# Kernel optimization log

Measured on AMD Instinct MI355X. Metric: run time of the kernel, lower is better.

The kernel has to match this reference:

```python
import jax, jax.numpy as jnp
import numpy as np

N = 50000      # nodes
E = 250000     # edges
NG = 2500      # graphs
H = 32         # atom_dim
ND = 32        # node feature dim
ED = 16        # edge feature dim
CONV_N = 3     # message passing steps
EMB_STEPS = 3  # Set2Set processing steps


def setup_inputs() -> dict:
    key = jax.random.key(0)
    ks = jax.random.split(key, 16)
    w = lambda k, shape, s=0.05: jax.random.normal(k, shape, jnp.float32) * s
    return {
        "x": jax.random.normal(ks[0], (N, ND), jnp.float32),
        "edge_index": jax.random.randint(ks[1], (2, E), 0, N),
        "edge_attr": jax.random.normal(ks[2], (E, ED), jnp.float32),
        "batch": jnp.sort(jax.random.randint(ks[3], (N,), 0, NG)),
        "lin_w": w(ks[4], (ND, H)), "lin_b": jnp.zeros((H,), jnp.float32),
        "e_w1": w(ks[5], (ED, 2 * H)), "e_b1": jnp.zeros((2 * H,), jnp.float32),
        "e_w2": w(ks[6], (2 * H, H * H)), "e_b2": jnp.zeros((H * H,), jnp.float32),
        "gru_w_ih": w(ks[7], (3 * H, H)), "gru_w_hh": w(ks[8], (3 * H, H)),
        "gru_b_ih": jnp.zeros((3 * H,), jnp.float32), "gru_b_hh": jnp.zeros((3 * H,), jnp.float32),
        "lstm_w_ih": w(ks[9], (4 * H, 2 * H)), "lstm_w_hh": w(ks[10], (4 * H, H)),
        "lstm_b_ih": jnp.zeros((4 * H,), jnp.float32), "lstm_b_hh": jnp.zeros((4 * H,), jnp.float32),
        "pred_w": w(ks[11], (2 * H, 1)), "pred_b": jnp.zeros((1,), jnp.float32),
    }


def _mpnn_forward(x, edge_attr, lin_w, lin_b, e_w1, e_b1, e_w2, e_b2,
                  gru_w_ih, gru_w_hh, gru_b_ih, gru_b_hh,
                  lstm_w_ih, lstm_w_hh, lstm_b_ih, lstm_b_hh,
                  pred_w, pred_b, edge_index, batch):
    src, dst = edge_index[0], edge_index[1]
    # initial node embedding: relu(Linear(node_dim -> atom_dim))
    out = jax.nn.relu(x @ lin_w + lin_b)            # [N, H]
    h = out                                         # GRU hidden state [N, H]

    # edge-conditioned weights (edge MLP output is constant across conv steps)
    e_h = jax.nn.relu(edge_attr @ e_w1 + e_b1)      # [E, 2H]
    W_e = (e_h @ e_w2 + e_b2).reshape(E, H, H)      # [E, H, H]

    # mean-aggregation denominator per target node
    deg = jax.ops.segment_sum(jnp.ones((E,), out.dtype), dst, num_segments=N)
    denom = jnp.maximum(deg, 1.0)[:, None]          # [N, 1]

    for _ in range(CONV_N):
        # NNConv message: m_e = x_src @ W_e, mean-scattered to dst
        msg = jnp.einsum('eh,eho->eo', out[src], W_e)                   # [E, H]
        agg = jax.ops.segment_sum(msg, dst, num_segments=N) / denom     # [N, H]
        m = jax.nn.relu(agg)
        # single GRU cell step (seq_len=1)
        gi = m @ gru_w_ih.T + gru_b_ih              # [N, 3H]
        gh = h @ gru_w_hh.T + gru_b_hh              # [N, 3H]
        i_r, i_z, i_n = jnp.split(gi, 3, axis=-1)
        h_r, h_z, h_n = jnp.split(gh, 3, axis=-1)
        r = jax.nn.sigmoid(i_r + h_r)
        z = jax.nn.sigmoid(i_z + h_z)
        n = jnp.tanh(i_n + r * h_n)
        h = (1.0 - z) * n + z * h
        out = h

    # Set2Set pooling over graphs (only last embedding used, residual='last')
    q_star = jnp.zeros((NG, 2 * H), out.dtype)
    hl = jnp.zeros((NG, H), out.dtype)
    cl = jnp.zeros((NG, H), out.dtype)
    for _ in range(EMB_STEPS):
        g = q_star @ lstm_w_ih.T + lstm_b_ih + hl @ lstm_w_hh.T + lstm_b_hh  # [NG, 4H]
        gi_, gf_, gg_, go_ = jnp.split(g, 4, axis=-1)
        i_g = jax.nn.sigmoid(gi_)
        f_g = jax.nn.sigmoid(gf_)
        g_g = jnp.tanh(gg_)
        o_g = jax.nn.sigmoid(go_)
        cl = f_g * cl + i_g * g_g
        hl = o_g * jnp.tanh(cl)
        q = hl                                       # [NG, H]
        e = jnp.sum(out * q[batch], axis=-1)         # [N]
        e_max = jax.ops.segment_max(e, batch, num_segments=NG)
        e_exp = jnp.exp(e - e_max[batch])
        e_den = jax.ops.segment_sum(e_exp, batch, num_segments=NG)
        a = e_exp / e_den[batch]                     # softmax within each graph
        r_pool = jax.ops.segment_sum(a[:, None] * out, batch, num_segments=NG)  # [NG, H]
        q_star = jnp.concatenate([q, r_pool], axis=-1)

    pred = q_star @ pred_w + pred_b                  # [NG, 1]
    return pred.reshape(-1)


def reference(x, edge_index, edge_attr, batch, lin_w, lin_b, e_w1, e_b1, e_w2, e_b2,
              gru_w_ih, gru_w_hh, gru_b_ih, gru_b_hh,
              lstm_w_ih, lstm_w_hh, lstm_b_ih, lstm_b_hh, pred_w, pred_b):
    return _mpnn_forward(x, edge_attr, lin_w, lin_b, e_w1, e_b1, e_w2, e_b2,
                         gru_w_ih, gru_w_hh, gru_b_ih, gru_b_hh,
                         lstm_w_ih, lstm_w_hh, lstm_b_ih, lstm_b_hh,
                         pred_w, pred_b, edge_index, batch)
```

## Files before the change

### kernel.cpp

```cpp
#include <hip/hip_runtime.h>
#include <hip/hip_bf16.h>

namespace {
constexpr int kN = 50000;
constexpr int kE = 250000;
constexpr int kG = 2500;
constexpr int NB = 16;

__device__ __forceinline__ float sigmoidf_(float x) { return 1.0f / (1.0f + expf(-x)); }

__global__ void k_starts(const int* __restrict__ batch, int* __restrict__ starts) {
  int g = blockIdx.x * blockDim.x + threadIdx.x;
  if (g > kG) return;
  int lo = 0, hi = kN;
  while (lo < hi) {
    int mid = (lo + hi) >> 1;
    if (batch[mid] < g) lo = mid + 1; else hi = mid;
  }
  starts[g] = lo;
}

__global__ __launch_bounds__(256) void k_node_init(const float* __restrict__ x,
                                                   const float* __restrict__ lin_w,
                                                   const float* __restrict__ lin_b,
                                                   float* __restrict__ h) {
  __shared__ float ws[32 * 32];
  __shared__ float bs[32];
  for (int i = threadIdx.x; i < 1024; i += 256) ws[i] = lin_w[i];
  if (threadIdx.x < 32) bs[threadIdx.x] = lin_b[threadIdx.x];
  __syncthreads();
  int n = blockIdx.x * 256 + threadIdx.x;
  if (n >= kN) return;
  float xv[32];
  const float4* xp = (const float4*)(x + (size_t)n * 32);
#pragma unroll
  for (int i = 0; i < 8; ++i) {
    float4 v = xp[i];
    xv[4 * i + 0] = v.x; xv[4 * i + 1] = v.y; xv[4 * i + 2] = v.z; xv[4 * i + 3] = v.w;
  }
  float acc[32];
#pragma unroll
  for (int o = 0; o < 32; ++o) acc[o] = bs[o];
  for (int i = 0; i < 32; ++i) {
    float a = xv[i];
    const float4* wr = (const float4*)&ws[i * 32];
#pragma unroll
    for (int o4 = 0; o4 < 8; ++o4) {
      float4 w = wr[o4];
      acc[4 * o4 + 0] = fmaf(a, w.x, acc[4 * o4 + 0]);
      acc[4 * o4 + 1] = fmaf(a, w.y, acc[4 * o4 + 1]);
      acc[4 * o4 + 2] = fmaf(a, w.z, acc[4 * o4 + 2]);
      acc[4 * o4 + 3] = fmaf(a, w.w, acc[4 * o4 + 3]);
    }
  }
  float4* hp = (float4*)(h + (size_t)n * 32);
#pragma unroll
  for (int i = 0; i < 8; ++i) {
    float4 v;
    v.x = fmaxf(acc[4 * i + 0], 0.f);
    v.y = fmaxf(acc[4 * i + 1], 0.f);
    v.z = fmaxf(acc[4 * i + 2], 0.f);
    v.w = fmaxf(acc[4 * i + 3], 0.f);
    hp[i] = v;
  }
}

__global__ __launch_bounds__(256) void k_edge_h(const float* __restrict__ ea,
                                                const float* __restrict__ w1,
                                                const float* __restrict__ b1,
                                                float* __restrict__ eh) {
  __shared__ float ws[16 * 64];
  __shared__ float bs[64];
  for (int i = threadIdx.x; i < 1024; i += 256) ws[i] = w1[i];
  if (threadIdx.x < 64) bs[threadIdx.x] = b1[threadIdx.x];
  __syncthreads();
  int e = blockIdx.x * 256 + threadIdx.x;
  if (e >= kE) return;
  float av[16];
  const float4* ap = (const float4*)(ea + (size_t)e * 16);
#pragma unroll
  for (int i = 0; i < 4; ++i) {
    float4 v = ap[i];
    av[4 * i + 0] = v.x; av[4 * i + 1] = v.y; av[4 * i + 2] = v.z; av[4 * i + 3] = v.w;
  }
  float acc[64];
#pragma unroll
  for (int o = 0; o < 64; ++o) acc[o] = bs[o];
  for (int i = 0; i < 16; ++i) {
    float a = av[i];
    const float4* wr = (const float4*)&ws[i * 64];
#pragma unroll
    for (int o4 = 0; o4 < 16; ++o4) {
      float4 w = wr[o4];
      acc[4 * o4 + 0] = fmaf(a, w.x, acc[4 * o4 + 0]);
      acc[4 * o4 + 1] = fmaf(a, w.y, acc[4 * o4 + 1]);
      acc[4 * o4 + 2] = fmaf(a, w.z, acc[4 * o4 + 2]);
      acc[4 * o4 + 3] = fmaf(a, w.w, acc[4 * o4 + 3]);
    }
  }
  float4* op = (float4*)(eh + (size_t)e * 64);
#pragma unroll
  for (int i = 0; i < 16; ++i) {
    float4 v;
    v.x = fmaxf(acc[4 * i + 0], 0.f);
    v.y = fmaxf(acc[4 * i + 1], 0.f);
    v.z = fmaxf(acc[4 * i + 2], 0.f);
    v.w = fmaxf(acc[4 * i + 3], 0.f);
    op[i] = v;
  }
}

__global__ void k_deg_hist(const int* __restrict__ dst, const int* __restrict__ src,
                           float* __restrict__ denom, int* __restrict__ cnt) {
  int e = blockIdx.x * blockDim.x + threadIdx.x;
  if (e < kE) {
    atomicAdd(&denom[dst[e]], 1.0f);
    atomicAdd(&cnt[src[e]], 1);
  }
}

__global__ __launch_bounds__(1024) void k_scan(const int* __restrict__ cnt, int* __restrict__ offs) {
  __shared__ int wsum[16];
  __shared__ int wpre[16];
  __shared__ int carry_s;
  const int tid = threadIdx.x;
  const int lane = tid & 63, wv = tid >> 6;
  if (tid == 0) carry_s = 0;
  __syncthreads();
  for (int base = 0; base < kN; base += 1024) {
    int i = base + tid;
    int v = (i < kN) ? cnt[i] : 0;
    int x = v;
#pragma unroll
    for (int d = 1; d < 64; d <<= 1) {
      int t = __shfl_up(x, d, 64);
      if (lane >= d) x += t;
    }
    if (lane == 63) wsum[wv] = x;
    __syncthreads();
    if (wv == 0) {
      int y = (lane < 16) ? wsum[lane] : 0;
#pragma unroll
      for (int d = 1; d < 16; d <<= 1) {
        int t = __shfl_up(y, d, 64);
        if (lane >= d && lane < 16) y += t;
      }
      if (lane < 16) wpre[lane] = y - wsum[lane];
    }
    __syncthreads();
    int carry = carry_s;
    if (i < kN) offs[i] = carry + wpre[wv] + (x - v);
    __syncthreads();
    if (tid == 0) carry_s = carry + wpre[15] + wsum[15];
    __syncthreads();
  }
  if (tid == 0) offs[kN] = carry_s;
}

__global__ void k_scatter(const int* __restrict__ src, const int* __restrict__ dst,
                          const int* __restrict__ offs, int* __restrict__ cur,
                          int* __restrict__ es_e, int* __restrict__ es_src,
                          int* __restrict__ es_dst) {
  int e = blockIdx.x * blockDim.x + threadIdx.x;
  if (e >= kE) return;
  int s = src[e];
  int pos = offs[s] + atomicAdd(&cur[s], 1);
  es_e[pos] = e;
  es_src[pos] = s;
  es_dst[pos] = dst[e];
}

__global__ void k_w2t(const float* __restrict__ w2, float* __restrict__ w2t) {
  int i = blockIdx.x * 256 + threadIdx.x;
  if (i >= 65536) return;
  int k = i & 63, oa = i >> 6;
  int o = oa & 31, a = oa >> 5;
  w2t[i] = w2[(size_t)k * 1024 + a * 32 + o];
}

__global__ __launch_bounds__(256, 2) void k_conv2(const float* __restrict__ h,
                                                  const float* __restrict__ eh,
                                                  const float* __restrict__ w2t,
                                                  const float* __restrict__ b2,
                                                  const int* __restrict__ es_e,
                                                  const int* __restrict__ es_src,
                                                  const int* __restrict__ es_dst,
                                                  const int* __restrict__ offs,
                                                  float* __restrict__ agg) {
  __shared__ float Ts[NB][32][36];
  __shared__ float hs[NB][32];
  __shared__ float hb2[NB][32];
  const int n0 = blockIdx.x * NB;
  const int t = threadIdx.x;
  {
    int n = t >> 5, o = t & 31;
    hs[n][o]     = h[(size_t)(n0 + n) * 32 + o];
    hs[n + 8][o] = h[(size_t)(n0 + n + 8) * 32 + o];
  }
  __syncthreads();
  {
    int n = t >> 5, o = t & 31;
    float a0 = 0.f, a1 = 0.f;
    for (int a = 0; a < 32; ++a) {
      float b = b2[a * 32 + o];
      a0 = fmaf(hs[n][a], b, a0);
      a1 = fmaf(hs[n + 8][a], b, a1);
    }
    hb2[n][o] = a0;
    hb2[n + 8][o] = a1;
  }
  const int og = t >> 3;
  const int kq = t & 7;
  const int kg = t >> 5;
  const int ol = t & 31;
  const int es = offs[n0], ee = offs[n0 + NB];
  const float* wp = w2t + og * 64 + kq * 4;

  for (int kh = 0; kh < 2; ++kh) {
    float4 acc[NB];
#pragma unroll
    for (int n = 0; n < NB; ++n) acc[n] = make_float4(0.f, 0.f, 0.f, 0.f);
    const float* wph = wp + kh * 32;
    for (int a4 = 0; a4 < 8; ++a4) {
      const float* wa = wph + (size_t)(a4 * 4) * 2048;
      float4 w0 = *(const float4*)(wa);
      float4 w1 = *(const float4*)(wa + 2048);
      float4 w2v = *(const float4*)(wa + 4096);
      float4 w3 = *(const float4*)(wa + 6144);
#pragma unroll
      for (int n = 0; n < NB; ++n) {
        float4 hv = *(const float4*)&hs[n][a4 * 4];
        acc[n].x = fmaf(hv.x, w0.x, acc[n].x); acc[n].y = fmaf(hv.x, w0.y, acc[n].y);
        acc[n].z = fmaf(hv.x, w0.z, acc[n].z); acc[n].w = fmaf(hv.x, w0.w, acc[n].w);
        acc[n].x = fmaf(hv.y, w1.x, acc[n].x); acc[n].y = fmaf(hv.y, w1.y, acc[n].y);
        acc[n].z = fmaf(hv.y, w1.z, acc[n].z); acc[n].w = fmaf(hv.y, w1.w, acc[n].w);
        acc[n].x = fmaf(hv.z, w2v.x, acc[n].x); acc[n].y = fmaf(hv.z, w2v.y, acc[n].y);
        acc[n].z = fmaf(hv.z, w2v.z, acc[n].z); acc[n].w = fmaf(hv.z, w2v.w, acc[n].w);
        acc[n].x = fmaf(hv.w, w3.x, acc[n].x); acc[n].y = fmaf(hv.w, w3.y, acc[n].y);
        acc[n].z = fmaf(hv.w, w3.z, acc[n].z); acc[n].w = fmaf(hv.w, w3.w, acc[n].w);
      }
    }
    if (kh) __syncthreads();
#pragma unroll
    for (int n = 0; n < NB; ++n) *(float4*)&Ts[n][og][kq * 4] = acc[n];
    __syncthreads();
    for (int ei = es + kg; ei < ee; ei += 8) {
      const int e = es_e[ei];
      const int nl = es_src[ei] - n0;
      const int d = es_dst[ei];
      const float ehv = eh[(size_t)e * 64 + kh * 32 + ol];
      float m = kh ? 0.f : hb2[nl][ol];
      const float* tp = &Ts[nl][ol][0];
#pragma unroll
      for (int j4 = 0; j4 < 8; ++j4) {
        float4 tv = *(const float4*)(tp + j4 * 4);
        m = fmaf(__shfl(ehv, j4 * 4 + 0, 32), tv.x, m);
        m = fmaf(__shfl(ehv, j4 * 4 + 1, 32), tv.y, m);
        m = fmaf(__shfl(ehv, j4 * 4 + 2, 32), tv.z, m);
        m = fmaf(__shfl(ehv, j4 * 4 + 3, 32), tv.w, m);
      }
      atomicAdd(&agg[(size_t)d * 32 + ol], m);
    }
  }
}

__global__ __launch_bounds__(256) void k_gru(float* __restrict__ h, const float* __restrict__ agg,
                                             const float* __restrict__ denom,
                                             const float* __restrict__ Wih, const float* __restrict__ Whh,
                                             const float* __restrict__ bih, const float* __restrict__ bhh) {
  __shared__ float wih_s[96 * 32];
  __shared__ float whh_s[96 * 32];
  __shared__ float bih_s[96], bhh_s[96];
  for (int i = threadIdx.x; i < 96 * 32; i += 256) { wih_s[i] = Wih[i]; whh_s[i] = Whh[i]; }
  for (int i = threadIdx.x; i < 96; i += 256) { bih_s[i] = bih[i]; bhh_s[i] = bhh[i]; }
  __syncthreads();
  int n = blockIdx.x * 256 + threadIdx.x;
  if (n >= kN) return;
  float dn = fmaxf(denom[n], 1.0f);
  float m[32], hv[32];
  const float4* ap = (const float4*)(agg + (size_t)n * 32);
  const float4* hp = (const float4*)(h + (size_t)n * 32);
#pragma unroll
  for (int i = 0; i < 8; ++i) {
    float4 a = ap[i];
    m[4 * i + 0] = fmaxf(a.x / dn, 0.f);
    m[4 * i + 1] = fmaxf(a.y / dn, 0.f);
    m[4 * i + 2] = fmaxf(a.z / dn, 0.f);
    m[4 * i + 3] = fmaxf(a.w / dn, 0.f);
    float4 b = hp[i];
    hv[4 * i + 0] = b.x; hv[4 * i + 1] = b.y; hv[4 * i + 2] = b.z; hv[4 * i + 3] = b.w;
  }
  float rr[32], zz[32];
#pragma unroll 4
  for (int j = 0; j < 32; ++j) {
    float accA = bih_s[j], accB = bhh_s[j];
    const float4* wi = (const float4*)&wih_s[j * 32];
    const float4* wh = (const float4*)&whh_s[j * 32];
#pragma unroll
    for (int i = 0; i < 8; ++i) {
      float4 a = wi[i], b = wh[i];
      accA = fmaf(m[4 * i + 0], a.x, accA); accA = fmaf(m[4 * i + 1], a.y, accA);
      accA = fmaf(m[4 * i + 2], a.z, accA); accA = fmaf(m[4 * i + 3], a.w, accA);
      accB = fmaf(hv[4 * i + 0], b.x, accB); accB = fmaf(hv[4 * i + 1], b.y, accB);
      accB = fmaf(hv[4 * i + 2], b.z, accB); accB = fmaf(hv[4 * i + 3], b.w, accB);
    }
    rr[j] = sigmoidf_(accA + accB);
  }
#pragma unroll 4
  for (int j = 0; j < 32; ++j) {
    int row = 32 + j;
    float accA = bih_s[row], accB = bhh_s[row];
    const float4* wi = (const float4*)&wih_s[row * 32];
    const float4* wh = (const float4*)&whh_s[row * 32];
#pragma unroll
    for (int i = 0; i < 8; ++i) {
      float4 a = wi[i], b = wh[i];
      accA = fmaf(m[4 * i + 0], a.x, accA); accA = fmaf(m[4 * i + 1], a.y, accA);
      accA = fmaf(m[4 * i + 2], a.z, accA); accA = fmaf(m[4 * i + 3], a.w, accA);
      accB = fmaf(hv[4 * i + 0], b.x, accB); accB = fmaf(hv[4 * i + 1], b.y, accB);
      accB = fmaf(hv[4 * i + 2], b.z, accB); accB = fmaf(hv[4 * i + 3], b.w, accB);
    }
    zz[j] = sigmoidf_(accA + accB);
  }
#pragma unroll 4
  for (int j = 0; j < 32; ++j) {
    int row = 64 + j;
    float accA = bih_s[row], accB = bhh_s[row];
    const float4* wi = (const float4*)&wih_s[row * 32];
    const float4* wh = (const float4*)&whh_s[row * 32];
#pragma unroll
    for (int i = 0; i < 8; ++i) {
      float4 a = wi[i], b = wh[i];
      accA = fmaf(m[4 * i + 0], a.x, accA); accA = fmaf(m[4 * i + 1], a.y, accA);
      accA = fmaf(m[4 * i + 2], a.z, accA); accA = fmaf(m[4 * i + 3], a.w, accA);
      accB = fmaf(hv[4 * i + 0], b.x, accB); accB = fmaf(hv[4 * i + 1], b.y, accB);
      accB = fmaf(hv[4 * i + 2], b.z, accB); accB = fmaf(hv[4 * i + 3], b.w, accB);
    }
    float ng = tanhf(accA + rr[j] * accB);
    zz[j] = (1.f - zz[j]) * ng + zz[j] * hv[j];
  }
  float4* hw = (float4*)(h + (size_t)n * 32);
#pragma unroll
  for (int i = 0; i < 8; ++i)
    hw[i] = make_float4(zz[4 * i + 0], zz[4 * i + 1], zz[4 * i + 2], zz[4 * i + 3]);
}

__global__ __launch_bounds__(256) void k_s2s(const float* __restrict__ h,
                                             const int* __restrict__ starts,
                                             const float* __restrict__ lwih,
                                             const float* __restrict__ lwhh,
                                             const float* __restrict__ lbih,
                                             const float* __restrict__ lbhh,
                                             const float* __restrict__ pw,
                                             const float* __restrict__ pb,
                                             float* __restrict__ out) {
  __shared__ float wih_s[128][65];
  __shared__ float whh_s[128][33];
  __shared__ float bsum[128];
  for (int i = threadIdx.x; i < 128 * 64; i += 256) wih_s[i >> 6][i & 63] = lwih[i];
  for (int i = threadIdx.x; i < 128 * 32; i += 256) whh_s[i >> 5][i & 31] = lwhh[i];
  for (int i = threadIdx.x; i < 128; i += 256) bsum[i] = lbih[i] + lbhh[i];
  __syncthreads();
  const int g = blockIdx.x * 4 + (threadIdx.x >> 6);
  if (g >= kG) return;
  const int lane = threadIdx.x & 63;
  const int o = lane & 31;
  const int r1 = lane, r2 = lane + 64;
  const int s = starts[g], e = starts[g + 1];
  float c = 0.f, hl = 0.f, rp = 0.f;
  for (int step = 0; step < 3; ++step) {
    float v1 = bsum[r1], v2 = bsum[r2];
    for (int i = 0; i < 32; ++i) {
      float hli = __shfl(hl, i, 64);
      float rpi = __shfl(rp, i, 64);
      v1 = fmaf(wih_s[r1][i], hli, v1);
      v1 = fmaf(wih_s[r1][32 + i], rpi, v1);
      v1 = fmaf(whh_s[r1][i], hli, v1);
      v2 = fmaf(wih_s[r2][i], hli, v2);
      v2 = fmaf(wih_s[r2][32 + i], rpi, v2);
      v2 = fmaf(whh_s[r2][i], hli, v2);
    }
    float fg = sigmoidf_(__shfl(v1, 32 + o, 64));
    float og_ = sigmoidf_(__shfl(v2, 32 + o, 64));
    float ig = sigmoidf_(v1);
    float gg = tanhf(v2);
    c = fg * c + ig * gg;
    hl = og_ * tanhf(c);
    float q = __shfl(hl, o, 64);
    float mx = -3.0e38f;
    for (int nn = s; nn < e; nn += 2) {
      int n = nn + (lane >> 5);
      float val = (n < e) ? h[(size_t)n * 32 + o] * q : 0.f;
#pragma unroll
      for (int d = 16; d; d >>= 1) val += __shfl_xor(val, d, 32);
      if (n < e) mx = fmaxf(mx, val);
    }
    mx = fmaxf(mx, __shfl_xor(mx, 32, 64));
    float den = 0.f, racc = 0.f;
    for (int nn = s; nn < e; nn += 2) {
      int n = nn + (lane >> 5);
      float hvo = 0.f, val = 0.f;
      if (n < e) { hvo = h[(size_t)n * 32 + o]; val = hvo * q; }
#pragma unroll
      for (int d = 16; d; d >>= 1) val += __shfl_xor(val, d, 32);
      if (n < e) { float p = expf(val - mx); den += p; racc = fmaf(p, hvo, racc); }
    }
    den += __shfl_xor(den, 32, 64);
    racc += __shfl_xor(racc, 32, 64);
    rp = (e > s) ? racc / den : 0.f;
  }
  float acc = __shfl(hl, o, 64) * pw[o] + rp * pw[32 + o];
#pragma unroll
  for (int d = 16; d; d >>= 1) acc += __shfl_xor(acc, d, 32);
  if (lane == 0) out[g] = acc + pb[0];
}

}

extern "C" void kernel_launch(void* const* d_in, const int* in_sizes, int n_in,
                              void* d_out, int out_size, void* d_ws, size_t ws_size,
                              hipStream_t stream) {
  const float* x     = (const float*)d_in[0];
  const int*   eidx  = (const int*)d_in[1];
  const float* eattr = (const float*)d_in[2];
  const int*   batch = (const int*)d_in[3];
  const float* lin_w = (const float*)d_in[4];
  const float* lin_b = (const float*)d_in[5];
  const float* e_w1  = (const float*)d_in[6];
  const float* e_b1  = (const float*)d_in[7];
  const float* e_w2  = (const float*)d_in[8];
  const float* e_b2  = (const float*)d_in[9];
  const float* gwih  = (const float*)d_in[10];
  const float* gwhh  = (const float*)d_in[11];
  const float* gbih  = (const float*)d_in[12];
  const float* gbhh  = (const float*)d_in[13];
  const float* lwih  = (const float*)d_in[14];
  const float* lwhh  = (const float*)d_in[15];
  const float* lbih  = (const float*)d_in[16];
  const float* lbhh  = (const float*)d_in[17];
  const float* pw    = (const float*)d_in[18];
  const float* pb    = (const float*)d_in[19];
  const int* srcp = eidx;
  const int* dstp = eidx + kE;

  float* ws = (float*)d_ws;
  size_t off = 0;
  auto alloc = [&](size_t nel) {
    float* p = ws + off;
    off += (nel + 255) & ~(size_t)255;
    return p;
  };
  float* hbuf  = alloc((size_t)kN * 32);
  float* agg   = alloc((size_t)kN * 32);
  float* denom = alloc(kN);
  float* ehb   = alloc((size_t)kE * 64);
  float* w2t   = alloc(65536);
  int* starts  = (int*)alloc(kG + 1);
  int* cnt     = (int*)alloc(kN);
  int* cur     = (int*)alloc(kN);
  int* offs    = (int*)alloc(kN + 1);
  int* es_e    = (int*)alloc(kE);
  int* es_src  = (int*)alloc(kE);
  int* es_dst  = (int*)alloc(kE);
  if (ws_size / 4 < off) return;

  hipMemsetAsync(denom, 0, (size_t)kN * 4, stream);
  hipMemsetAsync(cnt, 0, (size_t)kN * 4, stream);
  hipMemsetAsync(cur, 0, (size_t)kN * 4, stream);

  k_starts<<<(kG + 1 + 255) / 256, 256, 0, stream>>>(batch, starts);
  k_node_init<<<(kN + 255) / 256, 256, 0, stream>>>(x, lin_w, lin_b, hbuf);
  k_edge_h<<<(kE + 255) / 256, 256, 0, stream>>>(eattr, e_w1, e_b1, ehb);
  k_deg_hist<<<(kE + 255) / 256, 256, 0, stream>>>(dstp, srcp, denom, cnt);
  k_scan<<<1, 1024, 0, stream>>>(cnt, offs);
  k_scatter<<<(kE + 255) / 256, 256, 0, stream>>>(srcp, dstp, offs, cur, es_e, es_src, es_dst);
  k_w2t<<<65536 / 256, 256, 0, stream>>>(e_w2, w2t);

  for (int step = 0; step < 3; ++step) {
    hipMemsetAsync(agg, 0, (size_t)kN * 32 * 4, stream);
    k_conv2<<<kN / NB, 256, 0, stream>>>(hbuf, ehb, w2t, e_b2, es_e, es_src, es_dst, offs, agg);
    k_gru<<<(kN + 255) / 256, 256, 0, stream>>>(hbuf, agg, denom, gwih, gwhh, gbih, gbhh);
  }

  k_s2s<<<(kG + 3) / 4, 256, 0, stream>>>(hbuf, starts, lwih, lwhh, lbih, lbhh, pw, pb,
                                          (float*)d_out);
}
```

Baseline: 1.099 ms.

## Replace atomic scatter-add with per-edge message buffer and CSR gather by destination

```diff
diff --git a/kernel.cpp b/kernel.cpp
--- a/kernel.cpp
+++ b/kernel.cpp
@@ -5,7 +5,7 @@
 constexpr int kN = 50000;
 constexpr int kE = 250000;
 constexpr int kG = 2500;
-constexpr int NB = 16;
+constexpr int NB = 8;
 
 __device__ __forceinline__ float sigmoidf_(float x) { return 1.0f / (1.0f + expf(-x)); }
 
@@ -68,7 +68,8 @@
 __global__ __launch_bounds__(256) void k_edge_h(const float* __restrict__ ea,
                                                 const float* __restrict__ w1,
                                                 const float* __restrict__ b1,
-                                                float* __restrict__ eh) {
+                                                const int* __restrict__ pos_of_e,
+                                                float* __restrict__ ehs) {
   __shared__ float ws[16 * 64];
   __shared__ float bs[64];
   for (int i = threadIdx.x; i < 1024; i += 256) ws[i] = w1[i];
@@ -98,7 +99,7 @@
       acc[4 * o4 + 3] = fmaf(a, w.w, acc[4 * o4 + 3]);
     }
   }
-  float4* op = (float4*)(eh + (size_t)e * 64);
+  float4* op = (float4*)(ehs + (size_t)pos_of_e[e] * 64);
 #pragma unroll
   for (int i = 0; i < 16; ++i) {
     float4 v;
@@ -110,16 +111,19 @@
   }
 }
 
-__global__ void k_deg_hist(const int* __restrict__ dst, const int* __restrict__ src,
-                           float* __restrict__ denom, int* __restrict__ cnt) {
+__global__ void k_hist2(const int* __restrict__ src, const int* __restrict__ dst,
+                        int* __restrict__ cnt_s, int* __restrict__ cnt_d) {
   int e = blockIdx.x * blockDim.x + threadIdx.x;
   if (e < kE) {
-    atomicAdd(&denom[dst[e]], 1.0f);
-    atomicAdd(&cnt[src[e]], 1);
-  }
-}
-
-__global__ __launch_bounds__(1024) void k_scan(const int* __restrict__ cnt, int* __restrict__ offs) {
+    atomicAdd(&cnt_s[src[e]], 1);
+    atomicAdd(&cnt_d[dst[e]], 1);
+  }
+}
+
+__global__ __launch_bounds__(1024) void k_scan2(const int* __restrict__ cnt_s, int* __restrict__ offs_s,
+                                                const int* __restrict__ cnt_d, int* __restrict__ offs_d) {
+  const int* cnt = blockIdx.x ? cnt_d : cnt_s;
+  int* offs = blockIdx.x ? offs_d : offs_s;
   __shared__ int wsum[16];
   __shared__ int wpre[16];
   __shared__ int carry_s;
@@ -157,17 +161,26 @@
   if (tid == 0) offs[kN] = carry_s;
 }
 
-__global__ void k_scatter(const int* __restrict__ src, const int* __restrict__ dst,
-                          const int* __restrict__ offs, int* __restrict__ cur,
-                          int* __restrict__ es_e, int* __restrict__ es_src,
-                          int* __restrict__ es_dst) {
+__global__ void k_scatter_s(const int* __restrict__ src, const int* __restrict__ dst,
+                            const int* __restrict__ offs, int* __restrict__ cur,
+                            unsigned char* __restrict__ es_nl, int* __restrict__ es_dst,
+                            int* __restrict__ pos_of_e) {
   int e = blockIdx.x * blockDim.x + threadIdx.x;
   if (e >= kE) return;
   int s = src[e];
   int pos = offs[s] + atomicAdd(&cur[s], 1);
-  es_e[pos] = e;
-  es_src[pos] = s;
+  es_nl[pos] = (unsigned char)(s & (NB - 1));
   es_dst[pos] = dst[e];
+  pos_of_e[e] = pos;
+}
+
+__global__ void k_scatter_d(const int* __restrict__ es_dst, const int* __restrict__ offs_d,
+                            int* __restrict__ cur_d, int* __restrict__ ed_pos) {
+  int ei = blockIdx.x * blockDim.x + threadIdx.x;
+  if (ei >= kE) return;
+  int d = es_dst[ei];
+  int pd = offs_d[d] + atomicAdd(&cur_d[d], 1);
+  ed_pos[pd] = ei;
 }
 
 __global__ void k_w2t(const float* __restrict__ w2, float* __restrict__ w2t) {
@@ -178,41 +191,29 @@
   w2t[i] = w2[(size_t)k * 1024 + a * 32 + o];
 }
 
-__global__ __launch_bounds__(256, 2) void k_conv2(const float* __restrict__ h,
-                                                  const float* __restrict__ eh,
+__global__ __launch_bounds__(256, 4) void k_conv3(const float* __restrict__ h,
+                                                  const float* __restrict__ ehs,
                                                   const float* __restrict__ w2t,
                                                   const float* __restrict__ b2,
-                                                  const int* __restrict__ es_e,
-                                                  const int* __restrict__ es_src,
-                                                  const int* __restrict__ es_dst,
+                                                  const unsigned char* __restrict__ es_nl,
                                                   const int* __restrict__ offs,
-                                                  float* __restrict__ agg) {
+                                                  float* __restrict__ msgbuf) {
   __shared__ float Ts[NB][32][36];
   __shared__ float hs[NB][32];
   __shared__ float hb2[NB][32];
   const int n0 = blockIdx.x * NB;
   const int t = threadIdx.x;
-  {
-    int n = t >> 5, o = t & 31;
-    hs[n][o]     = h[(size_t)(n0 + n) * 32 + o];
-    hs[n + 8][o] = h[(size_t)(n0 + n + 8) * 32 + o];
-  }
+  const int nloc = t >> 5, o32 = t & 31;
+  hs[nloc][o32] = h[(size_t)(n0 + nloc) * 32 + o32];
   __syncthreads();
   {
-    int n = t >> 5, o = t & 31;
-    float a0 = 0.f, a1 = 0.f;
-    for (int a = 0; a < 32; ++a) {
-      float b = b2[a * 32 + o];
-      a0 = fmaf(hs[n][a], b, a0);
-      a1 = fmaf(hs[n + 8][a], b, a1);
-    }
-    hb2[n][o] = a0;
-    hb2[n + 8][o] = a1;
+    float a0 = 0.f;
+#pragma unroll 8
+    for (int a = 0; a < 32; ++a) a0 = fmaf(hs[nloc][a], b2[a * 32 + o32], a0);
+    hb2[nloc][o32] = a0;
   }
   const int og = t >> 3;
   const int kq = t & 7;
-  const int kg = t >> 5;
-  const int ol = t & 31;
   const int es = offs[n0], ee = offs[n0 + NB];
   const float* wp = w2t + og * 64 + kq * 4;
 
@@ -221,6 +222,7 @@
 #pragma unroll
     for (int n = 0; n < NB; ++n) acc[n] = make_float4(0.f, 0.f, 0.f, 0.f);
     const float* wph = wp + kh * 32;
+#pragma unroll 2
     for (int a4 = 0; a4 < 8; ++a4) {
       const float* wa = wph + (size_t)(a4 * 4) * 2048;
       float4 w0 = *(const float4*)(wa);
@@ -244,13 +246,13 @@
 #pragma unroll
     for (int n = 0; n < NB; ++n) *(float4*)&Ts[n][og][kq * 4] = acc[n];
     __syncthreads();
+    const int kg = t >> 5;
+#pragma unroll 2
     for (int ei = es + kg; ei < ee; ei += 8) {
-      const int e = es_e[ei];
-      const int nl = es_src[ei] - n0;
-      const int d = es_dst[ei];
-      const float ehv = eh[(size_t)e * 64 + kh * 32 + ol];
-      float m = kh ? 0.f : hb2[nl][ol];
-      const float* tp = &Ts[nl][ol][0];
+      const int nl = es_nl[ei];
+      const float ehv = ehs[(size_t)ei * 64 + kh * 32 + o32];
+      float m = kh ? msgbuf[(size_t)ei * 32 + o32] : hb2[nl][o32];
+      const float* tp = &Ts[nl][o32][0];
 #pragma unroll
       for (int j4 = 0; j4 < 8; ++j4) {
         float4 tv = *(const float4*)(tp + j4 * 4);
@@ -259,13 +261,32 @@
         m = fmaf(__shfl(ehv, j4 * 4 + 2, 32), tv.z, m);
         m = fmaf(__shfl(ehv, j4 * 4 + 3, 32), tv.w, m);
       }
-      atomicAdd(&agg[(size_t)d * 32 + ol], m);
-    }
-  }
-}
-
-__global__ __launch_bounds__(256) void k_gru(float* __restrict__ h, const float* __restrict__ agg,
-                                             const float* __restrict__ denom,
+      msgbuf[(size_t)ei * 32 + o32] = m;
+    }
+  }
+}
+
+__global__ __launch_bounds__(256) void k_agg(const float* __restrict__ msgbuf,
+                                             const int* __restrict__ ed_pos,
+                                             const int* __restrict__ offs_d,
+                                             float* __restrict__ m_out) {
+  int d = blockIdx.x * 8 + (threadIdx.x >> 5);
+  if (d >= kN) return;
+  int o = threadIdx.x & 31;
+  int s = offs_d[d], e = offs_d[d + 1];
+  float acc = 0.f;
+  int j = s;
+  for (; j + 1 < e; j += 2) {
+    int p0 = ed_pos[j], p1 = ed_pos[j + 1];
+    acc += msgbuf[(size_t)p0 * 32 + o] + msgbuf[(size_t)p1 * 32 + o];
+  }
+  if (j < e) acc += msgbuf[(size_t)ed_pos[j] * 32 + o];
+  float dn = (float)(e - s);
+  if (dn < 1.f) dn = 1.f;
+  m_out[(size_t)d * 32 + o] = fmaxf(acc / dn, 0.f);
+}
+
+__global__ __launch_bounds__(256) void k_gru(float* __restrict__ h, const float* __restrict__ m_in,
                                              const float* __restrict__ Wih, const float* __restrict__ Whh,
                                              const float* __restrict__ bih, const float* __restrict__ bhh) {
   __shared__ float wih_s[96 * 32];
@@ -276,17 +297,13 @@
   __syncthreads();
   int n = blockIdx.x * 256 + threadIdx.x;
   if (n >= kN) return;
-  float dn = fmaxf(denom[n], 1.0f);
   float m[32], hv[32];
-  const float4* ap = (const float4*)(agg + (size_t)n * 32);
+  const float4* ap = (const float4*)(m_in + (size_t)n * 32);
   const float4* hp = (const float4*)(h + (size_t)n * 32);
 #pragma unroll
   for (int i = 0; i < 8; ++i) {
     float4 a = ap[i];
-    m[4 * i + 0] = fmaxf(a.x / dn, 0.f);
-    m[4 * i + 1] = fmaxf(a.y / dn, 0.f);
-    m[4 * i + 2] = fmaxf(a.z / dn, 0.f);
-    m[4 * i + 3] = fmaxf(a.w / dn, 0.f);
+    m[4 * i + 0] = a.x; m[4 * i + 1] = a.y; m[4 * i + 2] = a.z; m[4 * i + 3] = a.w;
     float4 b = hp[i];
     hv[4 * i + 0] = b.x; hv[4 * i + 1] = b.y; hv[4 * i + 2] = b.z; hv[4 * i + 3] = b.w;
   }
@@ -450,36 +467,43 @@
     off += (nel + 255) & ~(size_t)255;
     return p;
   };
-  float* hbuf  = alloc((size_t)kN * 32);
-  float* agg   = alloc((size_t)kN * 32);
-  float* denom = alloc(kN);
-  float* ehb   = alloc((size_t)kE * 64);
-  float* w2t   = alloc(65536);
-  int* starts  = (int*)alloc(kG + 1);
-  int* cnt     = (int*)alloc(kN);
-  int* cur     = (int*)alloc(kN);
-  int* offs    = (int*)alloc(kN + 1);
-  int* es_e    = (int*)alloc(kE);
-  int* es_src  = (int*)alloc(kE);
-  int* es_dst  = (int*)alloc(kE);
+  float* hbuf   = alloc((size_t)kN * 32);
+  float* mbuf   = alloc((size_t)kN * 32);
+  float* ehs    = alloc((size_t)kE * 64);
+  float* msgbuf = alloc((size_t)kE * 32);
+  float* w2t    = alloc(65536);
+  int* starts   = (int*)alloc(kG + 1);
+  int* cnt_s    = (int*)alloc(kN);
+  int* cnt_d    = (int*)alloc(kN);
+  int* cur_s    = (int*)alloc(kN);
+  int* cur_d    = (int*)alloc(kN);
+  int* offs_s   = (int*)alloc(kN + 1);
+  int* offs_d   = (int*)alloc(kN + 1);
+  int* es_dst   = (int*)alloc(kE);
+  int* pos_of_e = (int*)alloc(kE);
+  int* ed_pos   = (int*)alloc(kE);
+  unsigned char* es_nl = (unsigned char*)alloc((kE + 3) / 4);
   if (ws_size / 4 < off) return;
 
-  hipMemsetAsync(denom, 0, (size_t)kN * 4, stream);
-  hipMemsetAsync(cnt, 0, (size_t)kN * 4, stream);
-  hipMemsetAsync(cur, 0, (size_t)kN * 4, stream);
+  hipMemsetAsync(cnt_s, 0, (size_t)kN * 4, stream);
+  hipMemsetAsync(cnt_d, 0, (size_t)kN * 4, stream);
+  hipMemsetAsync(cur_s, 0, (size_t)kN * 4, stream);
+  hipMemsetAsync(cur_d, 0, (size_t)kN * 4, stream);
 
   k_starts<<<(kG + 1 + 255) / 256, 256, 0, stream>>>(batch, starts);
   k_node_init<<<(kN + 255) / 256, 256, 0, stream>>>(x, lin_w, lin_b, hbuf);
-  k_edge_h<<<(kE + 255) / 256, 256, 0, stream>>>(eattr, e_w1, e_b1, ehb);
-  k_deg_hist<<<(kE + 255) / 256, 256, 0, stream>>>(dstp, srcp, denom, cnt);
-  k_scan<<<1, 1024, 0, stream>>>(cnt, offs);
-  k_scatter<<<(kE + 255) / 256, 256, 0, stream>>>(srcp, dstp, offs, cur, es_e, es_src, es_dst);
+  k_hist2<<<(kE + 255) / 256, 256, 0, stream>>>(srcp, dstp, cnt_s, cnt_d);
+  k_scan2<<<2, 1024, 0, stream>>>(cnt_s, offs_s, cnt_d, offs_d);
+  k_scatter_s<<<(kE + 255) / 256, 256, 0, stream>>>(srcp, dstp, offs_s, cur_s, es_nl, es_dst,
+                                                    pos_of_e);
+  k_edge_h<<<(kE + 255) / 256, 256, 0, stream>>>(eattr, e_w1, e_b1, pos_of_e, ehs);
+  k_scatter_d<<<(kE + 255) / 256, 256, 0, stream>>>(es_dst, offs_d, cur_d, ed_pos);
   k_w2t<<<65536 / 256, 256, 0, stream>>>(e_w2, w2t);
 
   for (int step = 0; step < 3; ++step) {
-    hipMemsetAsync(agg, 0, (size_t)kN * 32 * 4, stream);
-    k_conv2<<<kN / NB, 256, 0, stream>>>(hbuf, ehb, w2t, e_b2, es_e, es_src, es_dst, offs, agg);
-    k_gru<<<(kN + 255) / 256, 256, 0, stream>>>(hbuf, agg, denom, gwih, gwhh, gbih, gbhh);
+    k_conv3<<<kN / NB, 256, 0, stream>>>(hbuf, ehs, w2t, e_b2, es_nl, offs_s, msgbuf);
+    k_agg<<<(kN + 7) / 8, 256, 0, stream>>>(msgbuf, ed_pos, offs_d, mbuf);
+    k_gru<<<(kN + 255) / 256, 256, 0, stream>>>(hbuf, mbuf, gwih, gwhh, gbih, gbhh);
   }
 
   k_s2s<<<(kG + 3) / 4, 256, 0, stream>>>(hbuf, starts, lwih, lwhh, lbih, lbhh, pw, pb,
```

Measured after the change: 1.004 ms. 8.6% less time.
